# Kernel optimization log

Measured on AMD Instinct MI355X. Metric: run time of the kernel, lower is better.

## Reference

```python
import jax, jax.numpy as jnp
import numpy as np

ALPHA = 0.2  # LeakyReLU negative slope
NEG_INF = -9e15


def make_quaternion_mul(kernel):
    # kernel: (in/4, out); returns hamilton: (in, out)
    r, i, j, k = jnp.split(kernel, 4, axis=1)
    r2 = jnp.concatenate([r, -i, -j, -k], axis=0)
    i2 = jnp.concatenate([i, r, -k, j], axis=0)
    j2 = jnp.concatenate([j, k, r, -i], axis=0)
    k2 = jnp.concatenate([k, -j, i, r], axis=0)
    return jnp.concatenate([r2, i2, j2, k2], axis=1)


def setup_inputs() -> dict:
    key = jax.random.key(0)
    k1, k2, k3, k4 = jax.random.split(key, 4)
    N, IN, OUT, H = 4096, 512, 128, 4
    x = jax.random.normal(k1, (N, IN), dtype=jnp.float32)
    adj = jax.random.randint(k2, (N, N), 0, 2, dtype=jnp.int32)
    stdv = float(np.sqrt(6.0 / (IN // 4 + OUT)))
    W = jax.random.uniform(k3, (H, IN // 4, OUT), dtype=jnp.float32,
                           minval=-stdv, maxval=stdv)
    a_std = float(np.sqrt(2.0 / (2 * OUT + 1))) * 1.414
    a = jax.random.normal(k4, (H, 2 * OUT), dtype=jnp.float32) * a_std
    return {"x": x, "adj": adj, "W": W, "a": a}


def reference(x, adj, W, a):
    N = x.shape[0]
    hamilton = jax.vmap(make_quaternion_mul)(W)          # (H, IN, OUT)
    h = jnp.einsum('nf,hfo->hno', x, hamilton)           # (H, N, OUT)
    OUT = h.shape[-1]
    a_src, a_dst = a[:, :OUT], a[:, OUT:]
    # e[h,i,j] = leakyrelu(h_i . a_src + h_j . a_dst), same math as repeat/cat
    f_src = jnp.einsum('hno,ho->hn', h, a_src)           # (H, N)
    f_dst = jnp.einsum('hno,ho->hn', h, a_dst)           # (H, N)
    e = jax.nn.leaky_relu(f_src[:, :, None] + f_dst[:, None, :], ALPHA)
    e = jnp.where((adj > 0)[None, :, :], e, NEG_INF)
    attn = jax.nn.softmax(e, axis=-1)                    # (H, N, N)
    # dropout p=0.0 / eval mode -> identity
    h_prime = jnp.einsum('hnm,hmo->hno', attn, h)        # (H, N, OUT)
    out = jnp.transpose(h_prime, (1, 0, 2)).reshape(N, -1)  # concat heads
    return jax.nn.elu(out)
```

## Files before the change

kernel.cpp:

```cpp
#include <hip/hip_runtime.h>
#include <math.h>

#define ALPHA 0.2f

#define XS   544
#define HS   4128
#define HCS  66048

typedef __attribute__((ext_vector_type(8))) short short8;
typedef __attribute__((ext_vector_type(4))) float f32x4;
typedef __attribute__((ext_vector_type(4))) int i32x4;

__device__ __forceinline__ unsigned short f2bf(float f) {
    unsigned int x = __float_as_uint(f);
    x += 0x7fffu + ((x >> 16) & 1u);
    return (unsigned short)(x >> 16);
}
__device__ __forceinline__ unsigned int pack_rne(float lo, float hi) {
    return (unsigned int)f2bf(lo) | ((unsigned int)f2bf(hi) << 16);
}
__device__ __forceinline__ unsigned int pack_trunc(float lo, float hi) {
    return __builtin_amdgcn_perm(__float_as_uint(hi), __float_as_uint(lo), 0x07060302u);
}
__device__ __forceinline__ unsigned int bitmask1(unsigned int x, int j) {
    return (unsigned int)(((int)(x << (31 - j))) >> 31);
}

__global__ __launch_bounds__(256) void k_prep(const float* __restrict__ x,
                                              const float* __restrict__ W,
                                              const int* __restrict__ adj,
                                              unsigned short* __restrict__ xbf,
                                              unsigned short* __restrict__ hamT,
                                              unsigned int* __restrict__ adjp32) {
    const int b = blockIdx.x;
    if (b < 1024) {
        const int gid = b * 256 + threadIdx.x;
        const int row = gid >> 6, c8 = (gid & 63) * 8;
        const float4* xp = (const float4*)x + (size_t)gid * 2;
        const float4 f0 = xp[0], f1 = xp[1];
        const uint4 o = {pack_rne(f0.x, f0.y), pack_rne(f0.z, f0.w),
                         pack_rne(f1.x, f1.y), pack_rne(f1.z, f1.w)};
        *(uint4*)(xbf + (size_t)row * XS + c8) = o;
    } else if (b < 1152) {
        const int gid = (b - 1024) * 256 + threadIdx.x;
        const int head = gid >> 13;
        const int rem  = gid & 8191;
        const int o = rem >> 6, f8 = rem & 63;
        const int ob = o >> 5, oc = o & 31;
        float v[8];
#pragma unroll
        for (int j = 0; j < 8; j++) {
            const int f = f8 * 8 + j;
            const int bq = f >> 7, f0 = f & 127;
            const float s = ((0x5390u >> ((bq << 2) | ob)) & 1u) ? -1.0f : 1.0f;
            v[j] = s * W[(head << 14) + (f0 << 7) + (((bq ^ ob) << 5) | oc)];
        }
        const uint4 pk = {pack_rne(v[0], v[1]), pack_rne(v[2], v[3]),
                          pack_rne(v[4], v[5]), pack_rne(v[6], v[7])};
        *(uint4*)(hamT + (size_t)(head * 128 + o) * XS + f8 * 8) = pk;
    } else {
        const int gid = (b - 1152) * 256 + threadIdx.x;
        const int4* ap = (const int4*)(adj + (size_t)gid * 32);
        unsigned int u = 0;
#pragma unroll
        for (int q = 0; q < 8; q++) {
            const int4 v = ap[q];
            u |= (v.x > 0 ? 1u : 0u) << (q * 4);
            u |= (v.y > 0 ? 2u : 0u) << (q * 4);
            u |= (v.z > 0 ? 4u : 0u) << (q * 4);
            u |= (v.w > 0 ? 8u : 0u) << (q * 4);
        }
        adjp32[gid] = u;
    }
}

__global__ __launch_bounds__(256) void k_h(const unsigned short* __restrict__ xbf,
                                           const unsigned short* __restrict__ hamT,
                                           const float* __restrict__ a,
                                           unsigned short* __restrict__ hBT,
                                           float2* __restrict__ fsE,
                                           float2* __restrict__ fdE) {
    const int t = threadIdx.x;
    const int head = blockIdx.y;
    const int n0 = blockIdx.x * 64;
    const int wv = t >> 6, lane = t & 63;
    const int quad = lane >> 4, nl = lane & 15;
    const unsigned short* ap = xbf + (size_t)(n0 + wv * 16 + nl) * XS + quad * 8;
    const unsigned short* bp = hamT + (size_t)(head * 128 + nl) * XS + quad * 8;
    f32x4 acc[8];
#pragma unroll
    for (int ct = 0; ct < 8; ct++) acc[ct] = (f32x4){0.f, 0.f, 0.f, 0.f};
    for (int kc = 0; kc < 16; kc++) {
        const short8 af = *(const short8*)(ap + kc * 32);
#pragma unroll
        for (int ct = 0; ct < 8; ct++) {
            const short8 bf_ = *(const short8*)(bp + (size_t)ct * 16 * XS + kc * 32);
            acc[ct] = __builtin_amdgcn_mfma_f32_16x16x32_bf16(af, bf_, acc[ct], 0, 0, 0);
        }
    }
    const int rbase = n0 + wv * 16 + quad * 4;
#pragma unroll
    for (int ct = 0; ct < 8; ct++) {
        const uint2 pk = {pack_rne(acc[ct][0], acc[ct][1]), pack_rne(acc[ct][2], acc[ct][3])};
        *(uint2*)(hBT + (size_t)(head * 128 + ct * 16 + nl) * HS + rbase) = pk;
    }
    float fsr[4] = {0.f, 0.f, 0.f, 0.f}, fdr[4] = {0.f, 0.f, 0.f, 0.f};
#pragma unroll
    for (int ct = 0; ct < 8; ct++) {
        const int col = ct * 16 + nl;
        const float as = a[head * 256 + col];
        const float ad = a[head * 256 + 128 + col];
#pragma unroll
        for (int r = 0; r < 4; r++) {
            fsr[r] += acc[ct][r] * as;
            fdr[r] += acc[ct][r] * ad;
        }
    }
#pragma unroll
    for (int off = 1; off < 16; off <<= 1)
#pragma unroll
        for (int r = 0; r < 4; r++) {
            fsr[r] += __shfl_xor(fsr[r], off, 64);
            fdr[r] += __shfl_xor(fdr[r], off, 64);
        }
    if (nl == 0) {
#pragma unroll
        for (int r = 0; r < 4; r++) {
            const int n = rbase + r;
            fsE[(head << 12) + n] = make_float2(__expf(fsr[r]), __expf(ALPHA * fsr[r]));
            fdE[(head << 12) + n] = make_float2(__expf(fdr[r]), __expf(ALPHA * fdr[r]));
        }
    }
}

#define WELT(e1, ea, j, bits, es) \
    __uint_as_float(__float_as_uint(fmaxf((es).x * (e1), (es).y * (ea))) & bitmask1((bits), (j)))
#define WPK(f4, jb, bits, es) \
    pack_trunc(WELT((f4).x, (f4).y, (jb), (bits), (es)), \
               WELT((f4).z, (f4).w, (jb) + 1, (bits), (es)))

#define LOADM(S, mcn) do {                                                \
    const int _mo = (mcn) * 32;                                           \
    _Pragma("unroll")                                                     \
    for (int _ct = 0; _ct < 8; _ct++)                                     \
        Bst[S][_ct] = *(const short8*)(bbase + (size_t)_ct * HCS + _mo);  \
    _Pragma("unroll")                                                     \
    for (int _rt = 0; _rt < 4; _rt++) Kst[S][_rt] = ap[_rt][(mcn) * 4];   \
    _Pragma("unroll")                                                     \
    for (int _q = 0; _q < 4; _q++) Fst[S][_q] = fdb[(mcn) * 16 + _q];     \
} while (0)

#define EXECM(S) do {                                                     \
    short8 _af[4];                                                        \
    _Pragma("unroll")                                                     \
    for (int _rt = 0; _rt < 4; _rt++) {                                   \
        const i32x4 _ai = {(int)WPK(Fst[S][0], 0, Kst[S][_rt], es[_rt]),  \
                           (int)WPK(Fst[S][1], 2, Kst[S][_rt], es[_rt]),  \
                           (int)WPK(Fst[S][2], 4, Kst[S][_rt], es[_rt]),  \
                           (int)WPK(Fst[S][3], 6, Kst[S][_rt], es[_rt])}; \
        _af[_rt] = __builtin_bit_cast(short8, _ai);                       \
    }                                                                     \
    _Pragma("unroll")                                                     \
    for (int _rt = 0; _rt < 4; _rt++) {                                   \
        _Pragma("unroll")                                                 \
        for (int _ct = 0; _ct < 8; _ct++)                                 \
            acc[_rt][_ct] = __builtin_amdgcn_mfma_f32_16x16x32_bf16(      \
                _af[_rt], Bst[S][_ct], acc[_rt][_ct], 0, 0, 0);           \
        accL[_rt] = __builtin_amdgcn_mfma_f32_16x16x32_bf16(              \
            _af[_rt], ones, accL[_rt], 0, 0, 0);                          \
    }                                                                     \
} while (0)

__global__ __launch_bounds__(256, 1) void k_attn(const unsigned char* __restrict__ adjp,
                                                 const float2* __restrict__ fsE,
                                                 const float2* __restrict__ fdE,
                                                 const unsigned short* __restrict__ hBT,
                                                 float* __restrict__ out) {
    __shared__ f32x4 cbuf[1536];
    __shared__ f32x4 Lbuf[1024];
    const int t = threadIdx.x;
    const int head = blockIdx.x & 3;
    const int n0 = (blockIdx.x >> 2) * 64;
    const int wv = t >> 6, lane = t & 63;
    const int quad = lane >> 4, nl = lane & 15;
    const int m0base = wv << 10;
    float2 es[4];
    const unsigned char* ap[4];
#pragma unroll
    for (int rt = 0; rt < 4; rt++) {
        es[rt] = fsE[(head << 12) + n0 + rt * 16 + nl];
        ap[rt] = adjp + ((size_t)(n0 + rt * 16 + nl) << 9) + (m0base >> 3) + quad;
    }
    const float4* fdb = (const float4*)(fdE + (head << 12) + m0base + quad * 8);
    const unsigned short* bbase = hBT + (size_t)(head * 128 + nl) * HS + quad * 8 + m0base;
    const short8 ones = __builtin_bit_cast(short8,
        (i32x4){0x3F803F80, 0x3F803F80, 0x3F803F80, 0x3F803F80});
    f32x4 acc[4][8], accL[4];
#pragma unroll
    for (int rt = 0; rt < 4; rt++) {
        accL[rt] = (f32x4){0.f, 0.f, 0.f, 0.f};
#pragma unroll
        for (int ct = 0; ct < 8; ct++) acc[rt][ct] = (f32x4){0.f, 0.f, 0.f, 0.f};
    }
    short8 Bst[2][8];
    unsigned int Kst[2][4];
    float4 Fst[2][4];
    LOADM(0, 0);
    LOADM(1, 1);
    for (int mc = 0; mc < 32; mc += 2) {
        EXECM(0);
        LOADM(0, (mc + 2) & 31);
        EXECM(1);
        LOADM(1, (mc + 3) & 31);
    }
#pragma unroll
    for (int rt = 0; rt < 4; rt++) Lbuf[(wv * 4 + rt) * 64 + lane] = accL[rt];
#pragma unroll
    for (int rt = 0; rt < 4; rt++) {
        if (rt > 0) __syncthreads();
#pragma unroll
        for (int ct = 0; ct < 8; ct++) {
            const int owner = ct & 3;
            if (owner != wv) {
                const int j = (wv - owner - 1) & 3;
                cbuf[(ct * 3 + j) * 64 + lane] = acc[rt][ct];
            }
        }
        __syncthreads();
        f32x4 Lt = (f32x4){0.f, 0.f, 0.f, 0.f};
#pragma unroll
        for (int v = 0; v < 4; v++) Lt += Lbuf[(v * 4 + rt) * 64 + lane];
        float iL[4];
#pragma unroll
        for (int r = 0; r < 4; r++) iL[r] = (Lt[r] > 0.f) ? (1.0f / Lt[r]) : 0.0f;
#pragma unroll
        for (int ct = 0; ct < 8; ct++) {
            if ((ct & 3) == wv) {
                f32x4 tot = acc[rt][ct];
#pragma unroll
                for (int j = 0; j < 3; j++) tot += cbuf[(ct * 3 + j) * 64 + lane];
#pragma unroll
                for (int r = 0; r < 4; r++) {
                    float v = tot[r] * iL[r];
                    v = v > 0.f ? v : (__expf(v) - 1.0f);
                    out[(size_t)(n0 + rt * 16 + quad * 4 + r) * 512
                        + head * 128 + ct * 16 + nl] = v;
                }
            }
        }
    }
}

extern "C" void kernel_launch(void* const* d_in, const int* in_sizes, int n_in,
                              void* d_out, int out_size, void* d_ws, size_t ws_size,
                              hipStream_t stream) {
    (void)in_sizes; (void)n_in; (void)out_size; (void)ws_size;
    const float* x   = (const float*)d_in[0];
    const int*   adj = (const int*)d_in[1];
    const float* W   = (const float*)d_in[2];
    const float* a   = (const float*)d_in[3];
    float* out = (float*)d_out;

    char* ws = (char*)d_ws;
    unsigned short* xbf  = (unsigned short*)(ws);
    unsigned short* hBT  = (unsigned short*)(ws + 4456448);
    unsigned short* hamT = (unsigned short*)(ws + 8683520);
    unsigned char*  adjp = (unsigned char*)(ws + 9240576);
    float2*         fsE  = (float2*)(ws + 11337728);
    float2*         fdE  = (float2*)(ws + 11468800);

    hipLaunchKernelGGL(k_prep, dim3(3200),    dim3(256), 0, stream,
                       x, W, adj, xbf, hamT, (unsigned int*)adjp);
    hipLaunchKernelGGL(k_h,    dim3(64, 4),   dim3(256), 0, stream, xbf, hamT, a, hBT, fsE, fdE);
    hipLaunchKernelGGL(k_attn, dim3(256),     dim3(256), 0, stream, adjp, fsE, fdE, hBT, out);
}
```

Baseline: 160.0 us.

## Split attention work by rows per wave instead of key-range reduction

Each wave now handles its own 16 query rows over the full key range, where before four waves split the key dimension and reduced partial sums through shared memory. This removes the LDS reduction buffers and the block barriers. The adjacency bitmask is stored transposed by 32-column chunk so each lane fetches one word per chunk. The trade-off is that B-operand (h) loads are no longer shared across four row tiles, so each wave issues four times more h loads per MFMA, and the inner loop is four times longer.

```diff
diff --git a/kernel.cpp b/kernel.cpp
--- a/kernel.cpp
+++ b/kernel.cpp
@@ -31,7 +31,7 @@
                                               const int* __restrict__ adj,
                                               unsigned short* __restrict__ xbf,
                                               unsigned short* __restrict__ hamT,
-                                              unsigned int* __restrict__ adjp32) {
+                                              unsigned int* __restrict__ adjpT) {
     const int b = blockIdx.x;
     if (b < 1024) {
         const int gid = b * 256 + threadIdx.x;
@@ -60,7 +60,9 @@
         *(uint4*)(hamT + (size_t)(head * 128 + o) * XS + f8 * 8) = pk;
     } else {
         const int gid = (b - 1152) * 256 + threadIdx.x;
-        const int4* ap = (const int4*)(adj + (size_t)gid * 32);
+        const int mcch = gid >> 12;
+        const int row  = gid & 4095;
+        const int4* ap = (const int4*)(adj + (size_t)row * 4096 + mcch * 32);
         unsigned int u = 0;
 #pragma unroll
         for (int q = 0; q < 8; q++) {
@@ -70,7 +72,7 @@
             u |= (v.z > 0 ? 4u : 0u) << (q * 4);
             u |= (v.w > 0 ? 8u : 0u) << (q * 4);
         }
-        adjp32[gid] = u;
+        adjpT[gid] = u;
     }
 }
 
@@ -144,111 +146,68 @@
     _Pragma("unroll")                                                     \
     for (int _ct = 0; _ct < 8; _ct++)                                     \
         Bst[S][_ct] = *(const short8*)(bbase + (size_t)_ct * HCS + _mo);  \
-    _Pragma("unroll")                                                     \
-    for (int _rt = 0; _rt < 4; _rt++) Kst[S][_rt] = ap[_rt][(mcn) * 4];   \
+    Kst[S] = adjpT[(size_t)(mcn) * 4096 + rowIdx];                        \
     _Pragma("unroll")                                                     \
     for (int _q = 0; _q < 4; _q++) Fst[S][_q] = fdb[(mcn) * 16 + _q];     \
 } while (0)
 
 #define EXECM(S) do {                                                     \
-    short8 _af[4];                                                        \
+    const unsigned int _bits = (Kst[S] >> (quad * 8)) & 0xFFu;            \
+    const i32x4 _ai = {(int)WPK(Fst[S][0], 0, _bits, es),                 \
+                       (int)WPK(Fst[S][1], 2, _bits, es),                 \
+                       (int)WPK(Fst[S][2], 4, _bits, es),                 \
+                       (int)WPK(Fst[S][3], 6, _bits, es)};                \
+    const short8 _af = __builtin_bit_cast(short8, _ai);                   \
     _Pragma("unroll")                                                     \
-    for (int _rt = 0; _rt < 4; _rt++) {                                   \
-        const i32x4 _ai = {(int)WPK(Fst[S][0], 0, Kst[S][_rt], es[_rt]),  \
-                           (int)WPK(Fst[S][1], 2, Kst[S][_rt], es[_rt]),  \
-                           (int)WPK(Fst[S][2], 4, Kst[S][_rt], es[_rt]),  \
-                           (int)WPK(Fst[S][3], 6, Kst[S][_rt], es[_rt])}; \
-        _af[_rt] = __builtin_bit_cast(short8, _ai);                       \
-    }                                                                     \
-    _Pragma("unroll")                                                     \
-    for (int _rt = 0; _rt < 4; _rt++) {                                   \
-        _Pragma("unroll")                                                 \
-        for (int _ct = 0; _ct < 8; _ct++)                                 \
-            acc[_rt][_ct] = __builtin_amdgcn_mfma_f32_16x16x32_bf16(      \
-                _af[_rt], Bst[S][_ct], acc[_rt][_ct], 0, 0, 0);           \
-        accL[_rt] = __builtin_amdgcn_mfma_f32_16x16x32_bf16(              \
-            _af[_rt], ones, accL[_rt], 0, 0, 0);                          \
-    }                                                                     \
+    for (int _ct = 0; _ct < 8; _ct++)                                     \
+        acc[_ct] = __builtin_amdgcn_mfma_f32_16x16x32_bf16(               \
+            _af, Bst[S][_ct], acc[_ct], 0, 0, 0);                         \
+    accL = __builtin_amdgcn_mfma_f32_16x16x32_bf16(_af, ones, accL, 0, 0, 0); \
 } while (0)
 
-__global__ __launch_bounds__(256, 1) void k_attn(const unsigned char* __restrict__ adjp,
+__global__ __launch_bounds__(256, 1) void k_attn(const unsigned int* __restrict__ adjpT,
                                                  const float2* __restrict__ fsE,
                                                  const float2* __restrict__ fdE,
                                                  const unsigned short* __restrict__ hBT,
                                                  float* __restrict__ out) {
-    __shared__ f32x4 cbuf[1536];
-    __shared__ f32x4 Lbuf[1024];
     const int t = threadIdx.x;
     const int head = blockIdx.x & 3;
     const int n0 = (blockIdx.x >> 2) * 64;
     const int wv = t >> 6, lane = t & 63;
     const int quad = lane >> 4, nl = lane & 15;
-    const int m0base = wv << 10;
-    float2 es[4];
-    const unsigned char* ap[4];
-#pragma unroll
-    for (int rt = 0; rt < 4; rt++) {
-        es[rt] = fsE[(head << 12) + n0 + rt * 16 + nl];
-        ap[rt] = adjp + ((size_t)(n0 + rt * 16 + nl) << 9) + (m0base >> 3) + quad;
-    }
-    const float4* fdb = (const float4*)(fdE + (head << 12) + m0base + quad * 8);
-    const unsigned short* bbase = hBT + (size_t)(head * 128 + nl) * HS + quad * 8 + m0base;
+    const int rowIdx = n0 + wv * 16 + nl;
+    const float2 es = fsE[(head << 12) + rowIdx];
+    const float4* fdb = (const float4*)(fdE + (head << 12)) + quad * 4;
+    const unsigned short* bbase = hBT + (size_t)(head * 128 + nl) * HS + quad * 8;
     const short8 ones = __builtin_bit_cast(short8,
         (i32x4){0x3F803F80, 0x3F803F80, 0x3F803F80, 0x3F803F80});
-    f32x4 acc[4][8], accL[4];
-#pragma unroll
-    for (int rt = 0; rt < 4; rt++) {
-        accL[rt] = (f32x4){0.f, 0.f, 0.f, 0.f};
-#pragma unroll
-        for (int ct = 0; ct < 8; ct++) acc[rt][ct] = (f32x4){0.f, 0.f, 0.f, 0.f};
-    }
+    f32x4 acc[8];
+    f32x4 accL = (f32x4){0.f, 0.f, 0.f, 0.f};
+#pragma unroll
+    for (int ct = 0; ct < 8; ct++) acc[ct] = (f32x4){0.f, 0.f, 0.f, 0.f};
     short8 Bst[2][8];
-    unsigned int Kst[2][4];
+    unsigned int Kst[2];
     float4 Fst[2][4];
     LOADM(0, 0);
     LOADM(1, 1);
-    for (int mc = 0; mc < 32; mc += 2) {
+    for (int mc = 0; mc < 128; mc += 2) {
         EXECM(0);
-        LOADM(0, (mc + 2) & 31);
+        LOADM(0, (mc + 2) & 127);
         EXECM(1);
-        LOADM(1, (mc + 3) & 31);
-    }
-#pragma unroll
-    for (int rt = 0; rt < 4; rt++) Lbuf[(wv * 4 + rt) * 64 + lane] = accL[rt];
-#pragma unroll
-    for (int rt = 0; rt < 4; rt++) {
-        if (rt > 0) __syncthreads();
-#pragma unroll
-        for (int ct = 0; ct < 8; ct++) {
-            const int owner = ct & 3;
-            if (owner != wv) {
-                const int j = (wv - owner - 1) & 3;
-                cbuf[(ct * 3 + j) * 64 + lane] = acc[rt][ct];
-            }
-        }
-        __syncthreads();
-        f32x4 Lt = (f32x4){0.f, 0.f, 0.f, 0.f};
-#pragma unroll
-        for (int v = 0; v < 4; v++) Lt += Lbuf[(v * 4 + rt) * 64 + lane];
-        float iL[4];
-#pragma unroll
-        for (int r = 0; r < 4; r++) iL[r] = (Lt[r] > 0.f) ? (1.0f / Lt[r]) : 0.0f;
-#pragma unroll
-        for (int ct = 0; ct < 8; ct++) {
-            if ((ct & 3) == wv) {
-                f32x4 tot = acc[rt][ct];
-#pragma unroll
-                for (int j = 0; j < 3; j++) tot += cbuf[(ct * 3 + j) * 64 + lane];
-#pragma unroll
-                for (int r = 0; r < 4; r++) {
-                    float v = tot[r] * iL[r];
-                    v = v > 0.f ? v : (__expf(v) - 1.0f);
-                    out[(size_t)(n0 + rt * 16 + quad * 4 + r) * 512
-                        + head * 128 + ct * 16 + nl] = v;
-                }
-            }
-        }
-    }
+        LOADM(1, (mc + 3) & 127);
+    }
+    float iLv[4];
+#pragma unroll
+    for (int r = 0; r < 4; r++) iLv[r] = (accL[r] > 0.f) ? (1.0f / accL[r]) : 0.0f;
+#pragma unroll
+    for (int ct = 0; ct < 8; ct++)
+#pragma unroll
+        for (int r = 0; r < 4; r++) {
+            float v = acc[ct][r] * iLv[r];
+            v = v > 0.f ? v : (__expf(v) - 1.0f);
+            out[(size_t)(n0 + wv * 16 + quad * 4 + r) * 512
+                + head * 128 + ct * 16 + nl] = v;
+        }
 }
 
 extern "C" void kernel_launch(void* const* d_in, const int* in_sizes, int n_in,
@@ -265,12 +224,12 @@
     unsigned short* xbf  = (unsigned short*)(ws);
     unsigned short* hBT  = (unsigned short*)(ws + 4456448);
     unsigned short* hamT = (unsigned short*)(ws + 8683520);
-    unsigned char*  adjp = (unsigned char*)(ws + 9240576);
+    unsigned int*   adjpT= (unsigned int*)(ws + 9240576);
     float2*         fsE  = (float2*)(ws + 11337728);
     float2*         fdE  = (float2*)(ws + 11468800);
 
     hipLaunchKernelGGL(k_prep, dim3(3200),    dim3(256), 0, stream,
-                       x, W, adj, xbf, hamT, (unsigned int*)adjp);
+                       x, W, adj, xbf, hamT, adjpT);
     hipLaunchKernelGGL(k_h,    dim3(64, 4),   dim3(256), 0, stream, xbf, hamT, a, hBT, fsE, fdE);
-    hipLaunchKernelGGL(k_attn, dim3(256),     dim3(256), 0, stream, adjp, fsE, fdE, hBT, out);
-}
+    hipLaunchKernelGGL(k_attn, dim3(256),     dim3(256), 0, stream, adjpT, fsE, fdE, hBT, out);
+}
```

Result: slower. 216.4 us (+35.2%).
